# Kernel tuning notes

Measured on AMD Instinct MI355X. Metric: run time of the kernel, lower is better.

Reference implementation:

```python
import jax, jax.numpy as jnp
import numpy as np

B, N, F_IN, F_HID, F_OUT = 64, 1024, 64, 128, 64

def setup_inputs() -> dict:
    key = jax.random.key(0)
    ks = jax.random.split(key, 6)
    x = jax.random.normal(ks[0], (B, N, F_IN), dtype=jnp.float32)
    adj = jax.random.uniform(ks[1], (B, N, N), dtype=jnp.float32)
    mask = jax.random.randint(ks[2], (B, N), 0, 2).astype(bool)
    W1 = jax.random.normal(ks[3], (F_IN, F_HID), dtype=jnp.float32) * (1.0 / np.sqrt(F_IN))
    b1 = jnp.zeros((F_HID,), dtype=jnp.float32)
    W2 = jax.random.normal(ks[4], (F_HID, F_OUT), dtype=jnp.float32) * (1.0 / np.sqrt(F_HID))
    b2 = jnp.zeros((F_OUT,), dtype=jnp.float32)
    eps = jnp.zeros((1,), dtype=jnp.float32)
    return {"x": x, "adj": adj, "mask": mask, "W1": W1, "b1": b1, "W2": W2, "b2": b2, "eps": eps}

def reference(x, adj, mask, W1, b1, W2, b2, eps):
    # neighbor aggregation: out[b,i,f] = sum_j adj[b,i,j] * x[b,j,f]
    agg = jnp.einsum('bij,bjf->bif', adj, x)
    # add_loop=True: (1 + eps) * x + aggregated neighbors
    h = (1.0 + eps[0]) * x + agg
    # 2-layer GIN MLP applied per node (only valid nodes contribute in the
    # torch version via gather/scatter; invalid positions are zeroed)
    h = jax.nn.relu(h @ W1 + b1) @ W2 + b2
    return jnp.where(mask[..., None], h, jnp.zeros((), dtype=h.dtype))
```

## Files before the change

kernel.cpp:

```cpp
#include <hip/hip_runtime.h>


#define N_     1024
#define FIN    64
#define FHID   128
#define FOUT   64
#define HS_LD  68
#define H1_LD  132
#define FROW   17
#define NCHUNK 8
#define KSPC   8

typedef __attribute__((ext_vector_type(16))) float f32x16;
typedef __attribute__((ext_vector_type(8)))  short s16x8;
typedef __attribute__((ext_vector_type(4)))  short s16x4;

__device__ inline short f2bf(float f) {
    union { float f; unsigned int u; } v; v.f = f;
    unsigned int r = v.u + 0x7fffu + ((v.u >> 16) & 1u);
    return (short)(r >> 16);
}

__global__ __launch_bounds__(256) void xt_pack(const float* __restrict__ x,
                                               s16x8* __restrict__ xt)
{
    const int g  = blockIdx.x * 256 + threadIdx.x;
    const int n  = g & 31;
    const int ng = (g >> 5) & 1;
    const int ks = (g >> 6) & 63;
    const int b  = g >> 12;
    const int f  = ng * 32 + n;

    s16x8 u0, u1;
    #pragma unroll
    for (int k = 0; k < 8; ++k)
        u0[k] = f2bf(x[(size_t)(b * N_ + ks * 16 + k) * FIN + f]);
    #pragma unroll
    for (int k = 0; k < 8; ++k)
        u1[k] = f2bf(x[(size_t)(b * N_ + ks * 16 + 8 + k) * FIN + f]);
    xt[2 * g]     = u0;
    xt[2 * g + 1] = u1;
}

__global__ __launch_bounds__(256, 3) void gin_main(
    const float* __restrict__ x, const float* __restrict__ adj,
    const int* __restrict__ mask, const float* __restrict__ W1,
    const float* __restrict__ b1, const float* __restrict__ W2,
    const float* __restrict__ b2, const float* __restrict__ epsp,
    const s16x8* __restrict__ xt, float* __restrict__ out)
{
    __shared__ s16x8 region[2 * 64 * FROW];
    __shared__ float hs[64 * HS_LD];

    s16x8 (*asf)[64][FROW] = reinterpret_cast<s16x8 (*)[64][FROW]>(region);
    s16x4* asf4 = reinterpret_cast<s16x4*>(region);
    float* h1s = reinterpret_cast<float*>(region);

    const int t    = threadIdx.x;
    const int lane = t & 63;
    const int w    = t >> 6;
    const int b    = blockIdx.x >> 4;
    const int i0   = (blockIdx.x & 15) * 64;

    const float* xb   = x   + (size_t)b * N_ * FIN;
    const float* adjb = adj + (size_t)b * N_ * N_ + (size_t)i0 * N_;

    const int l31  = lane & 31;
    const int half = lane >> 5;
    const int mrow = (w & 1) * 32;
    const int ncol = (w >> 1) * 32;
    const int ngq  = (w >> 1);

    const int rq = t >> 5;
    const int cl = t & 31;
    const float* arow0 = adjb + (size_t)rq * N_ + cl * 4;

    const int bfl = l31 * 2 + half;
    const size_t bgbase = (size_t)(b * 64) * 2 + ngq;

    f32x16 acc;
    #pragma unroll
    for (int r = 0; r < 16; ++r) acc[r] = 0.f;

    float4 pa[8];
    s16x8  pbc[KSPC];
    s16x8  pbn[KSPC];

    #pragma unroll
    for (int q = 0; q < 8; ++q)
        pa[q] = *reinterpret_cast<const float4*>(arow0 + (size_t)q * 8 * N_);
    #pragma unroll
    for (int s = 0; s < KSPC; ++s)
        pbc[s] = xt[(bgbase + (size_t)(0 * KSPC + s) * 2) * 64 + bfl];
    #pragma unroll
    for (int q = 0; q < 8; ++q) {
        s16x4 fr;
        fr[0] = f2bf(pa[q].x); fr[1] = f2bf(pa[q].y);
        fr[2] = f2bf(pa[q].z); fr[3] = f2bf(pa[q].w);
        asf4[(q * 8 + rq) * 34 + cl] = fr;
    }
    __syncthreads();

    #pragma unroll
    for (int c = 0; c < NCHUNK; ++c) {
        if (c + 1 < NCHUNK) {
            #pragma unroll
            for (int q = 0; q < 8; ++q)
                pa[q] = *reinterpret_cast<const float4*>(arow0 + (size_t)q * 8 * N_ + (c + 1) * 128);
            #pragma unroll
            for (int s = 0; s < KSPC; ++s)
                pbn[s] = xt[(bgbase + (size_t)((c + 1) * KSPC + s) * 2) * 64 + bfl];
        }
        #pragma unroll
        for (int s = 0; s < KSPC; ++s) {
            const s16x8 a = asf[c & 1][mrow + l31][2 * s + half];
            acc = __builtin_amdgcn_mfma_f32_32x32x16_bf16(a, pbc[s], acc, 0, 0, 0);
        }
        if (c + 1 < NCHUNK) {
            const int boff = ((c + 1) & 1) * 2176;
            #pragma unroll
            for (int q = 0; q < 8; ++q) {
                s16x4 fr;
                fr[0] = f2bf(pa[q].x); fr[1] = f2bf(pa[q].y);
                fr[2] = f2bf(pa[q].z); fr[3] = f2bf(pa[q].w);
                asf4[boff + (q * 8 + rq) * 34 + cl] = fr;
            }
            #pragma unroll
            for (int s = 0; s < KSPC; ++s) pbc[s] = pbn[s];
            __syncthreads();
        }
    }

    {
        const float se = 1.0f + epsp[0];
        const int col = ncol + l31;
        #pragma unroll
        for (int reg = 0; reg < 16; ++reg) {
            const int row = mrow + (reg & 3) + 8 * (reg >> 2) + 4 * half;
            const float xv = xb[(size_t)(i0 + row) * FIN + col];
            hs[row * HS_LD + col] = acc[reg] + se * xv;
        }
    }
    __syncthreads();

    {
        const int k4 = (t & 31) * 4;
        const int rb = (t >> 5) * 8;
        float4 hacc[8];
        const float4 b1v = *reinterpret_cast<const float4*>(b1 + k4);
        #pragma unroll
        for (int r = 0; r < 8; ++r) hacc[r] = b1v;

        #pragma unroll 4
        for (int j = 0; j < FIN; ++j) {
            const float4 w1v = *reinterpret_cast<const float4*>(W1 + j * FHID + k4);
            #pragma unroll
            for (int r = 0; r < 8; ++r) {
                const float hv = hs[(rb + r) * HS_LD + j];
                hacc[r].x += hv * w1v.x; hacc[r].y += hv * w1v.y;
                hacc[r].z += hv * w1v.z; hacc[r].w += hv * w1v.w;
            }
        }
        #pragma unroll
        for (int r = 0; r < 8; ++r) {
            float4 v;
            v.x = fmaxf(hacc[r].x, 0.f); v.y = fmaxf(hacc[r].y, 0.f);
            v.z = fmaxf(hacc[r].z, 0.f); v.w = fmaxf(hacc[r].w, 0.f);
            *reinterpret_cast<float4*>(&h1s[(rb + r) * H1_LD + k4]) = v;
        }
    }
    __syncthreads();

    {
        const int fi = (t & 15) * 4;
        const int ri = (t >> 4) * 4;
        float4 oacc[4];
        const float4 b2v = *reinterpret_cast<const float4*>(b2 + fi);
        #pragma unroll
        for (int ii = 0; ii < 4; ++ii) oacc[ii] = b2v;

        #pragma unroll 4
        for (int j = 0; j < FHID; ++j) {
            const float4 w2v = *reinterpret_cast<const float4*>(W2 + j * FOUT + fi);
            #pragma unroll
            for (int ii = 0; ii < 4; ++ii) {
                const float hv = h1s[(ri + ii) * H1_LD + j];
                oacc[ii].x += hv * w2v.x; oacc[ii].y += hv * w2v.y;
                oacc[ii].z += hv * w2v.z; oacc[ii].w += hv * w2v.w;
            }
        }
        #pragma unroll
        for (int ii = 0; ii < 4; ++ii) {
            const int gi = i0 + ri + ii;
            const int m  = mask[b * N_ + gi];
            float4 o = oacc[ii];
            if (!m) o = make_float4(0.f, 0.f, 0.f, 0.f);
            *reinterpret_cast<float4*>(out + ((size_t)b * N_ + gi) * FOUT + fi) = o;
        }
    }
}

extern "C" void kernel_launch(void* const* d_in, const int* in_sizes, int n_in,
                              void* d_out, int out_size, void* d_ws, size_t ws_size,
                              hipStream_t stream) {
    const float* x    = (const float*)d_in[0];
    const float* adj  = (const float*)d_in[1];
    const int*   mask = (const int*)  d_in[2];
    const float* W1   = (const float*)d_in[3];
    const float* b1   = (const float*)d_in[4];
    const float* W2   = (const float*)d_in[5];
    const float* b2   = (const float*)d_in[6];
    const float* eps  = (const float*)d_in[7];
    float* out = (float*)d_out;
    s16x8* xt = (s16x8*)d_ws;

    xt_pack<<<dim3(1024), dim3(256), 0, stream>>>(x, xt);
    gin_main<<<dim3(64 * 16), dim3(256), 0, stream>>>(x, adj, mask, W1, b1, W2, b2, eps, xt, out);
}
```

Before: 418.3 us.

## Halve adj chunk size and prefetch two chunks ahead in register ring

The aggregation loop now processes 64-column chunks instead of 128, with a two-deep register ring that prefetches adj and packed x two chunks ahead, so global loads have more time to land before use. The full __syncthreads is replaced by an explicit LDS waitcnt plus s_barrier, letting outstanding global loads stay in flight across the barrier. The LDS tile gets a smaller padded stride. Twice as many barriers and smaller per-chunk MFMA batches are the trade-off, and register pressure may rise under the occupancy-3 launch bound.

```diff
diff --git a/kernel.cpp b/kernel.cpp
--- a/kernel.cpp
+++ b/kernel.cpp
@@ -7,9 +7,12 @@
 #define FOUT   64
 #define HS_LD  68
 #define H1_LD  132
-#define FROW   17
-#define NCHUNK 8
-#define KSPC   8
+#define CH     64
+#define NCHUNK 16
+#define KSPC   4
+#define FROW   9
+#define AUNITS 18
+#define BUFU   1152
 
 typedef __attribute__((ext_vector_type(16))) float f32x16;
 typedef __attribute__((ext_vector_type(8)))  short s16x8;
@@ -49,12 +52,12 @@
     const float* __restrict__ b2, const float* __restrict__ epsp,
     const s16x8* __restrict__ xt, float* __restrict__ out)
 {
-    __shared__ s16x8 region[2 * 64 * FROW];
+    __shared__ __align__(16) char region_raw[33792];
     __shared__ float hs[64 * HS_LD];
 
-    s16x8 (*asf)[64][FROW] = reinterpret_cast<s16x8 (*)[64][FROW]>(region);
-    s16x4* asf4 = reinterpret_cast<s16x4*>(region);
-    float* h1s = reinterpret_cast<float*>(region);
+    auto   asf  = reinterpret_cast<s16x8 (*)[64][FROW]>(region_raw);
+    s16x4* asf4 = reinterpret_cast<s16x4*>(region_raw);
+    float* h1s  = reinterpret_cast<float*>(region_raw);
 
     const int t    = threadIdx.x;
     const int lane = t & 63;
@@ -71,9 +74,9 @@
     const int ncol = (w >> 1) * 32;
     const int ngq  = (w >> 1);
 
-    const int rq = t >> 5;
-    const int cl = t & 31;
-    const float* arow0 = adjb + (size_t)rq * N_ + cl * 4;
+    const int rq16 = t >> 4;
+    const int cl16 = t & 15;
+    const float* adjA = adjb + (size_t)rq16 * N_ + cl16 * 4;
 
     const int bfl = l31 * 2 + half;
     const size_t bgbase = (size_t)(b * 64) * 2 + ngq;
@@ -82,52 +85,62 @@
     #pragma unroll
     for (int r = 0; r < 16; ++r) acc[r] = 0.f;
 
-    float4 pa[8];
-    s16x8  pbc[KSPC];
-    s16x8  pbn[KSPC];
-
-    #pragma unroll
-    for (int q = 0; q < 8; ++q)
-        pa[q] = *reinterpret_cast<const float4*>(arow0 + (size_t)q * 8 * N_);
+    float4 areg[2][4];
+    s16x8  xreg[2][4];
+
+    #pragma unroll
+    for (int q = 0; q < 4; ++q)
+        areg[0][q] = *reinterpret_cast<const float4*>(adjA + (size_t)q * 16 * N_);
+    #pragma unroll
+    for (int q = 0; q < 4; ++q)
+        areg[1][q] = *reinterpret_cast<const float4*>(adjA + (size_t)q * 16 * N_ + CH);
     #pragma unroll
     for (int s = 0; s < KSPC; ++s)
-        pbc[s] = xt[(bgbase + (size_t)(0 * KSPC + s) * 2) * 64 + bfl];
-    #pragma unroll
-    for (int q = 0; q < 8; ++q) {
+        xreg[0][s] = xt[(bgbase + (size_t)s * 2) * 64 + bfl];
+    #pragma unroll
+    for (int s = 0; s < KSPC; ++s)
+        xreg[1][s] = xt[(bgbase + (size_t)(KSPC + s) * 2) * 64 + bfl];
+
+    #pragma unroll
+    for (int q = 0; q < 4; ++q) {
         s16x4 fr;
-        fr[0] = f2bf(pa[q].x); fr[1] = f2bf(pa[q].y);
-        fr[2] = f2bf(pa[q].z); fr[3] = f2bf(pa[q].w);
-        asf4[(q * 8 + rq) * 34 + cl] = fr;
-    }
-    __syncthreads();
+        fr[0] = f2bf(areg[0][q].x); fr[1] = f2bf(areg[0][q].y);
+        fr[2] = f2bf(areg[0][q].z); fr[3] = f2bf(areg[0][q].w);
+        asf4[(q * 16 + rq16) * AUNITS + cl16] = fr;
+    }
+    asm volatile("s_waitcnt lgkmcnt(0)" ::: "memory");
+    __builtin_amdgcn_s_barrier();
 
     #pragma unroll
     for (int c = 0; c < NCHUNK; ++c) {
-        if (c + 1 < NCHUNK) {
-            #pragma unroll
-            for (int q = 0; q < 8; ++q)
-                pa[q] = *reinterpret_cast<const float4*>(arow0 + (size_t)q * 8 * N_ + (c + 1) * 128);
-            #pragma unroll
-            for (int s = 0; s < KSPC; ++s)
-                pbn[s] = xt[(bgbase + (size_t)((c + 1) * KSPC + s) * 2) * 64 + bfl];
+        if (c + 2 < NCHUNK) {
+            #pragma unroll
+            for (int q = 0; q < 4; ++q)
+                areg[c & 1][q] = *reinterpret_cast<const float4*>(
+                    adjA + (size_t)q * 16 * N_ + (size_t)(c + 2) * CH);
         }
         #pragma unroll
         for (int s = 0; s < KSPC; ++s) {
             const s16x8 a = asf[c & 1][mrow + l31][2 * s + half];
-            acc = __builtin_amdgcn_mfma_f32_32x32x16_bf16(a, pbc[s], acc, 0, 0, 0);
+            acc = __builtin_amdgcn_mfma_f32_32x32x16_bf16(a, xreg[c & 1][s], acc, 0, 0, 0);
+        }
+        if (c + 2 < NCHUNK) {
+            #pragma unroll
+            for (int s = 0; s < KSPC; ++s)
+                xreg[c & 1][s] = xt[(bgbase + (size_t)((c + 2) * KSPC + s) * 2) * 64 + bfl];
         }
         if (c + 1 < NCHUNK) {
-            const int boff = ((c + 1) & 1) * 2176;
-            #pragma unroll
-            for (int q = 0; q < 8; ++q) {
+            const int boff = ((c + 1) & 1) * BUFU;
+            #pragma unroll
+            for (int q = 0; q < 4; ++q) {
+                const float4 u = areg[(c + 1) & 1][q];
                 s16x4 fr;
-                fr[0] = f2bf(pa[q].x); fr[1] = f2bf(pa[q].y);
-                fr[2] = f2bf(pa[q].z); fr[3] = f2bf(pa[q].w);
-                asf4[boff + (q * 8 + rq) * 34 + cl] = fr;
+                fr[0] = f2bf(u.x); fr[1] = f2bf(u.y);
+                fr[2] = f2bf(u.z); fr[3] = f2bf(u.w);
+                asf4[boff + (q * 16 + rq16) * AUNITS + cl16] = fr;
             }
-            #pragma unroll
-            for (int s = 0; s < KSPC; ++s) pbc[s] = pbn[s];
-            __syncthreads();
+            asm volatile("s_waitcnt lgkmcnt(0)" ::: "memory");
+            __builtin_amdgcn_s_barrier();
         }
     }
 
```

Measured after the change: 422.9 us. Within noise of the previous version (+1.1%).
